# Kernel optimization log

Hardware: AMD Instinct MI355X
Metric: run time of the kernel (lower is better)

Reference implementation:

```python
import jax, jax.numpy as jnp
import numpy as np

N = 30000   # total nodes
E = 240000  # edges
B = 64      # graphs / proteins
H = 10      # GATv2 heads
C = 78      # per-head out dim (= xd_features)
D = H * C   # 780
SEQ = 1000
EMB = 128
LH = 64     # LSTM hidden per direction


def _lstm_dir(xs, Wih, Whh, bih, bhh, reverse):
    # xs: [T, Bn, EMB]; PyTorch gate order i,f,g,o
    Bn = xs.shape[1]
    h0 = jnp.zeros((Bn, LH), xs.dtype)
    def step(carry, xt):
        h, c = carry
        z = xt @ Wih.T + h @ Whh.T + bih + bhh
        i, f, g, o = jnp.split(z, 4, axis=-1)
        c = jax.nn.sigmoid(f) * c + jax.nn.sigmoid(i) * jnp.tanh(g)
        h = jax.nn.sigmoid(o) * jnp.tanh(c)
        return (h, c), h
    _, hs = jax.lax.scan(step, (h0, h0), xs, reverse=reverse)
    return hs


def setup_inputs() -> dict:
    k = jax.random.key(0)
    nxt = lambda i: jax.random.fold_in(k, i)
    s = 0.05
    d = {}
    d['x'] = jax.random.normal(nxt(0), (N, C), jnp.float32)
    d['edge_index'] = jax.random.randint(nxt(1), (2, E), 0, N)
    d['batch'] = jnp.sort(jax.random.randint(nxt(2), (N,), 0, B))
    d['target'] = jax.random.randint(nxt(3), (B, SEQ), 0, 26)
    # GATv2Conv params (share_weights=False)
    d['Wl'] = jax.random.normal(nxt(4), (C, D), jnp.float32) * s
    d['Wr'] = jax.random.normal(nxt(5), (C, D), jnp.float32) * s
    d['att'] = jax.random.normal(nxt(6), (H, C), jnp.float32) * s
    d['gat_b'] = jnp.zeros((D,), jnp.float32)
    # GCNConv params
    d['gcn_w'] = jax.random.normal(nxt(7), (D, D), jnp.float32) * s
    d['gcn_b'] = jnp.zeros((D,), jnp.float32)
    # protein branch
    d['emb'] = jax.random.normal(nxt(8), (26, EMB), jnp.float32) * s
    for tag, base in (('f', 9), ('b', 13)):
        d['Wih_' + tag] = jax.random.normal(nxt(base), (4 * LH, EMB), jnp.float32) * s
        d['Whh_' + tag] = jax.random.normal(nxt(base + 1), (4 * LH, LH), jnp.float32) * s
        d['bih_' + tag] = jnp.zeros((4 * LH,), jnp.float32)
        d['bhh_' + tag] = jnp.zeros((4 * LH,), jnp.float32)
    d['conv_w'] = jax.random.normal(nxt(17), (32, SEQ, 8), jnp.float32) * s
    d['conv_b'] = jnp.zeros((32,), jnp.float32)
    d['fcp_w'] = jax.random.normal(nxt(18), (32 * 121, 128), jnp.float32) * s
    d['fcp_b'] = jnp.zeros((128,), jnp.float32)
    # combined MLP (actual concat dim = 2*780 + 128 = 1688)
    d['fc1_w'] = jax.random.normal(nxt(19), (1688, 1024), jnp.float32) * s
    d['fc1_b'] = jnp.zeros((1024,), jnp.float32)
    d['fc2_w'] = jax.random.normal(nxt(20), (1024, 512), jnp.float32) * s
    d['fc2_b'] = jnp.zeros((512,), jnp.float32)
    d['out_w'] = jax.random.normal(nxt(21), (512, 1), jnp.float32) * s
    d['out_b'] = jnp.zeros((1,), jnp.float32)
    return d


def reference(x, edge_index, batch, target, Wl, Wr, att, gat_b, gcn_w, gcn_b,
              emb, Wih_f, Whh_f, bih_f, bhh_f, Wih_b, Whh_b, bih_b, bhh_b,
              conv_w, conv_b, fcp_w, fcp_b, fc1_w, fc1_b, fc2_w, fc2_b,
              out_w, out_b):
    # ---- graph branch (eval mode: dropout off) ----
    loops = jnp.arange(N)
    src = jnp.concatenate([edge_index[0], loops])  # self loops (PyG default)
    dst = jnp.concatenate([edge_index[1], loops])

    # GATv2Conv
    xl = (x @ Wl).reshape(N, H, C)
    xr = (x @ Wr).reshape(N, H, C)
    e = jax.nn.leaky_relu(xl[src] + xr[dst], 0.2)       # [E+N, H, C]
    logit = jnp.einsum('ehc,hc->eh', e, att)            # [E+N, H]
    m = jax.ops.segment_max(logit, dst, num_segments=N)
    ex = jnp.exp(logit - m[dst])
    den = jax.ops.segment_sum(ex, dst, num_segments=N)
    alpha = ex / den[dst]
    h = jax.ops.segment_sum(alpha[:, :, None] * xl[src], dst, num_segments=N)
    h = jax.nn.elu(h.reshape(N, D) + gat_b)

    # GCNConv with symmetric normalization
    hw = h @ gcn_w
    deg = jax.ops.segment_sum(jnp.ones_like(src, jnp.float32), dst, num_segments=N)
    dinv = jnp.where(deg > 0, jax.lax.rsqrt(jnp.maximum(deg, 1e-12)), 0.0)
    norm = dinv[src] * dinv[dst]
    g = jax.ops.segment_sum(norm[:, None] * hw[src], dst, num_segments=N) + gcn_b
    g = jax.nn.relu(g)

    # global max + mean pooling per graph
    gmax = jax.ops.segment_max(g, batch, num_segments=B)
    cnt = jax.ops.segment_sum(jnp.ones((N,), jnp.float32), batch, num_segments=B)
    gmean = jax.ops.segment_sum(g, batch, num_segments=B) / jnp.maximum(cnt, 1.0)[:, None]
    graph_feat = jnp.concatenate([gmax, gmean], axis=1)  # [B, 1560]

    # ---- protein branch ----
    et = emb[target]                                     # [B, SEQ, EMB]
    # nn.LSTM default batch_first=False: time axis is axis 0 (=B), batch axis is SEQ
    hf = _lstm_dir(et, Wih_f, Whh_f, bih_f, bhh_f, reverse=False)
    hb = _lstm_dir(et, Wih_b, Whh_b, bih_b, bhh_b, reverse=True)
    hcat = jnp.concatenate([hf, hb], axis=-1)            # [B, SEQ, 128]
    conv = jax.lax.conv_general_dilated(hcat, conv_w, (1,), 'VALID',
                                        dimension_numbers=('NCH', 'OIH', 'NCH'))
    conv = conv + conv_b[None, :, None]                  # [B, 32, 121]
    prot = conv.reshape(B, 32 * 121) @ fcp_w + fcp_b     # [B, 128]

    # ---- combined head ----
    comb = jnp.concatenate([graph_feat, prot], axis=1)   # [B, 1688]
    h1 = jax.nn.relu(comb @ fc1_w + fc1_b)
    h2 = jax.nn.relu(h1 @ fc2_w + fc2_b)
    return h2 @ out_w + out_b                            # [B, 1]
```

## Files before the change

### kernel.cpp

```cpp
#include <hip/hip_runtime.h>
#include <hip/hip_bf16.h>
#include <math.h>

static constexpr int NN   = 30000;
static constexpr int EE   = 240000;
static constexpr int ET   = EE + NN;
static constexpr int BB   = 64;
static constexpr int HH   = 10;
static constexpr int CC   = 78;
static constexpr int DD   = HH * CC;
static constexpr int SEQ  = 1000;
static constexpr int EMB  = 128;
static constexpr int LH   = 64;
static constexpr int COMBD = 2 * DD + 128;
static constexpr int PCHUNK = 64;

typedef __attribute__((ext_vector_type(8))) short short8;
typedef __attribute__((ext_vector_type(4))) float f32x4;

__device__ __forceinline__ float bf2f(unsigned short u) {
    return __uint_as_float(((unsigned int)u) << 16);
}

__device__ __forceinline__ float fast_sigmoid(float x) {
    return __builtin_amdgcn_rcpf(1.f + __expf(-x));
}
__device__ __forceinline__ float fast_tanh(float x) {
    float e = __expf(2.f * x);
    return 1.f - 2.f * __builtin_amdgcn_rcpf(e + 1.f);
}

template <int OBF>
__global__ __launch_bounds__(256) void gemm_bf16_mfma(const __hip_bfloat16* __restrict__ A,
                                                      const __hip_bfloat16* __restrict__ Bt,
                                                      void* __restrict__ Cv,
                                                      int M, int N, int K) {
    constexpr int LDS_S = 40;
    __shared__ unsigned short As[128 * LDS_S];
    __shared__ unsigned short Bs[128 * LDS_S];
    const int tid  = threadIdx.x;
    const int lane = tid & 63, wid = tid >> 6;
    const int wr = wid >> 1, wc = wid & 1;
    const int l15 = lane & 15, l4 = lane >> 4;
    int l = blockIdx.y * gridDim.x + blockIdx.x;
    {
        int nwg = gridDim.x * gridDim.y;
        int q = nwg >> 3, r = nwg & 7;
        int xcd = l & 7, idx = l >> 3;
        l = (xcd < r) ? (xcd * (q + 1) + idx) : (r * (q + 1) + (xcd - r) * q + idx);
    }
    const int bm = (l / gridDim.x) * 128;
    const int bn = (l % gridDim.x) * 128;
    const int tr = tid >> 2, tc = (tid & 3) * 8;

    const unsigned short* Au = (const unsigned short*)A;
    const unsigned short* Bu = (const unsigned short*)Bt;

    f32x4 acc[4][4];
#pragma unroll
    for (int m = 0; m < 4; ++m)
#pragma unroll
        for (int n = 0; n < 4; ++n) acc[m][n] = (f32x4){0.f, 0.f, 0.f, 0.f};

    for (int k0 = 0; k0 < K; k0 += 32) {
#pragma unroll
        for (int half = 0; half < 2; ++half) {
            int row = tr + half * 64;
            {
                int grow = bm + row;
                short8 sv;
                if (grow < M && k0 + tc + 8 <= K) {
                    const unsigned int* p = (const unsigned int*)(Au + (size_t)grow * K + k0 + tc);
#pragma unroll
                    for (int j = 0; j < 4; ++j) {
                        unsigned int u = p[j];
                        sv[2 * j]     = (short)(u & 0xffffu);
                        sv[2 * j + 1] = (short)(u >> 16);
                    }
                } else {
#pragma unroll
                    for (int j = 0; j < 8; ++j) {
                        int gk = k0 + tc + j;
                        sv[j] = (grow < M && gk < K) ? (short)Au[(size_t)grow * K + gk] : (short)0;
                    }
                }
                *reinterpret_cast<short8*>(&As[row * LDS_S + tc]) = sv;
            }
            {
                int grow = bn + row;
                short8 sv;
                if (grow < N && k0 + tc + 8 <= K) {
                    const unsigned int* p = (const unsigned int*)(Bu + (size_t)grow * K + k0 + tc);
#pragma unroll
                    for (int j = 0; j < 4; ++j) {
                        unsigned int u = p[j];
                        sv[2 * j]     = (short)(u & 0xffffu);
                        sv[2 * j + 1] = (short)(u >> 16);
                    }
                } else {
#pragma unroll
                    for (int j = 0; j < 8; ++j) {
                        int gk = k0 + tc + j;
                        sv[j] = (grow < N && gk < K) ? (short)Bu[(size_t)grow * K + gk] : (short)0;
                    }
                }
                *reinterpret_cast<short8*>(&Bs[row * LDS_S + tc]) = sv;
            }
        }
        __syncthreads();
        short8 a[4], b[4];
#pragma unroll
        for (int m = 0; m < 4; ++m)
            a[m] = *reinterpret_cast<const short8*>(&As[(wr * 64 + m * 16 + l15) * LDS_S + l4 * 8]);
#pragma unroll
        for (int n = 0; n < 4; ++n)
            b[n] = *reinterpret_cast<const short8*>(&Bs[(wc * 64 + n * 16 + l15) * LDS_S + l4 * 8]);
#pragma unroll
        for (int m = 0; m < 4; ++m)
#pragma unroll
            for (int n = 0; n < 4; ++n)
                acc[m][n] = __builtin_amdgcn_mfma_f32_16x16x32_bf16(a[m], b[n], acc[m][n], 0, 0, 0);
        __syncthreads();
    }
#pragma unroll
    for (int m = 0; m < 4; ++m)
#pragma unroll
        for (int n = 0; n < 4; ++n)
#pragma unroll
            for (int r = 0; r < 4; ++r) {
                int row = bm + wr * 64 + m * 16 + l4 * 4 + r;
                int col = bn + wc * 64 + n * 16 + l15;
                if (row < M && col < N) {
                    if (OBF)
                        ((__hip_bfloat16*)Cv)[(size_t)row * N + col] = __float2bfloat16(acc[m][n][r]);
                    else
                        ((float*)Cv)[(size_t)row * N + col] = acc[m][n][r];
                }
            }
}

__global__ void f32_to_bf16(const float* __restrict__ in, __hip_bfloat16* __restrict__ out, int n) {
    int i = blockIdx.x * blockDim.x + threadIdx.x;
    if (i < n) out[i] = __float2bfloat16(in[i]);
}

__global__ void transpose_to_bf16(const float* __restrict__ in, __hip_bfloat16* __restrict__ out,
                                  int Kdim, int Ndim) {
    int idx = blockIdx.x * blockDim.x + threadIdx.x;
    if (idx >= Kdim * Ndim) return;
    int n = idx / Kdim, k = idx % Kdim;
    out[idx] = __float2bfloat16(in[(size_t)k * Ndim + n]);
}

__global__ void transpose_f32(const float* __restrict__ in, float* __restrict__ out,
                              int Kdim, int Ndim) {
    int idx = blockIdx.x * blockDim.x + threadIdx.x;
    if (idx >= Kdim * Ndim) return;
    int n = idx / Kdim, k = idx % Kdim;
    out[idx] = in[(size_t)k * Ndim + n];
}

template <int ACT>
__global__ __launch_bounds__(256) void gemm_skinny(const float* __restrict__ A,
                                                   const float* __restrict__ Bt,
                                                   const float* __restrict__ bias,
                                                   float* __restrict__ C,
                                                   int M, int N, int K, int ldc) {
    int oidx = blockIdx.x * 4 + (threadIdx.x >> 6);
    int lane = threadIdx.x & 63;
    if (oidx >= M * N) return;
    int row = oidx / N, col = oidx % N;
    const float4* a = (const float4*)(A + (size_t)row * K);
    const float4* b = (const float4*)(Bt + (size_t)col * K);
    int K4 = K >> 2;
    float s = 0.f;
    for (int i = lane; i < K4; i += 64) {
        float4 x = a[i], y = b[i];
        s += x.x * y.x + x.y * y.y + x.z * y.z + x.w * y.w;
    }
#pragma unroll
    for (int off = 32; off; off >>= 1) s += __shfl_xor(s, off);
    if (lane == 0) {
        s += bias[col];
        if (ACT == 1) s = fmaxf(s, 0.f);
        C[(size_t)row * ldc + col] = s;
    }
}

__global__ void deg_count(const int* __restrict__ ei, int* __restrict__ deg) {
    int e = blockIdx.x * blockDim.x + threadIdx.x;
    if (e >= ET) return;
    int d = (e < EE) ? ei[EE + e] : (e - EE);
    atomicAdd(&deg[d], 1);
}

__global__ __launch_bounds__(1024) void scan_kernel(const int* __restrict__ deg,
                                                    int* __restrict__ offs) {
    __shared__ int lds[1024];
    int tid = threadIdx.x;
    const int chunk = (NN + 1023) / 1024;
    int base = tid * chunk;
    int s = 0;
    for (int i = 0; i < chunk; ++i) {
        int idx = base + i;
        if (idx < NN) s += deg[idx];
    }
    lds[tid] = s;
    __syncthreads();
    for (int d = 1; d < 1024; d <<= 1) {
        int v = (tid >= d) ? lds[tid - d] : 0;
        __syncthreads();
        lds[tid] += v;
        __syncthreads();
    }
    int run = (tid == 0) ? 0 : lds[tid - 1];
    for (int i = 0; i < chunk; ++i) {
        int idx = base + i;
        if (idx < NN) { offs[idx] = run; run += deg[idx]; }
    }
    if (tid == 1023) offs[NN] = lds[1023];
}

__global__ void csr_fill(const int* __restrict__ ei, const int* __restrict__ offs,
                         int* __restrict__ cursor, int* __restrict__ csr_src,
                         int* __restrict__ csr_dst) {
    int e = blockIdx.x * blockDim.x + threadIdx.x;
    if (e >= ET) return;
    int s = (e < EE) ? ei[e] : (e - EE);
    int d = (e < EE) ? ei[EE + e] : (e - EE);
    int pos = atomicAdd(&cursor[d], 1);
    int slot = offs[d] + pos;
    csr_src[slot] = s;
    csr_dst[slot] = d;
}

__global__ void dinv_kernel(const int* __restrict__ deg, float* __restrict__ dinv) {
    int n = blockIdx.x * blockDim.x + threadIdx.x;
    if (n >= NN) return;
    float dg = (float)deg[n];
    dinv[n] = (dg > 0.f) ? 1.f / sqrtf(dg) : 0.f;
}

__global__ void gat_logits(const unsigned short* __restrict__ xl,
                           const unsigned short* __restrict__ xr,
                           const float* __restrict__ att, const int* __restrict__ csr_src,
                           const int* __restrict__ csr_dst, float* __restrict__ logit) {
    int idx = blockIdx.x * blockDim.x + threadIdx.x;
    if (idx >= ET * HH) return;
    int i = idx / HH, h = idx % HH;
    int s = csr_src[i], d = csr_dst[i];
    const unsigned int* pl = (const unsigned int*)(xl + (size_t)s * DD + h * CC);
    const unsigned int* pr = (const unsigned int*)(xr + (size_t)d * DD + h * CC);
    const float* pa = att + h * CC;
    float acc = 0.f;
#pragma unroll
    for (int c = 0; c < CC / 2; ++c) {
        unsigned int a = pl[c], b = pr[c];
        float v0 = __uint_as_float((a & 0xffffu) << 16) + __uint_as_float((b & 0xffffu) << 16);
        float v1 = __uint_as_float(a & 0xffff0000u) + __uint_as_float(b & 0xffff0000u);
        v0 = (v0 > 0.f) ? v0 : 0.2f * v0;
        v1 = (v1 > 0.f) ? v1 : 0.2f * v1;
        acc += pa[2 * c] * v0 + pa[2 * c + 1] * v1;
    }
    logit[idx] = acc;
}

__global__ void gat_softmax(const int* __restrict__ offs, float* __restrict__ logit) {
    int idx = blockIdx.x * blockDim.x + threadIdx.x;
    if (idx >= NN * HH) return;
    int n = idx / HH, h = idx % HH;
    int i0 = offs[n], i1 = offs[n + 1];
    float m = -1e30f;
    for (int i = i0; i < i1; ++i) m = fmaxf(m, logit[i * HH + h]);
    float den = 0.f;
    for (int i = i0; i < i1; ++i) {
        float e = __expf(logit[i * HH + h] - m);
        logit[i * HH + h] = e;
        den += e;
    }
    float inv = __builtin_amdgcn_rcpf(den);
    for (int i = i0; i < i1; ++i) logit[i * HH + h] *= inv;
}

__global__ __launch_bounds__(256) void gat_aggregate(const int* __restrict__ offs,
                                                     const int* __restrict__ csr_src,
                                                     const float* __restrict__ alpha,
                                                     const unsigned short* __restrict__ xl,
                                                     const float* __restrict__ gat_b,
                                                     __hip_bfloat16* __restrict__ hout) {
    int n = blockIdx.x;
    int tid = threadIdx.x;
    int i0 = offs[n], i1 = offs[n + 1];
    int d0 = tid, d1 = tid + 256, d2 = tid + 512, d3 = tid + 768;
    int h0 = d0 / CC, h1 = d1 / CC, h2 = d2 / CC, h3 = (d3 < DD) ? d3 / CC : 0;
    float a0 = 0.f, a1 = 0.f, a2 = 0.f, a3 = 0.f;
    for (int i = i0; i < i1; ++i) {
        const unsigned short* row = xl + (size_t)csr_src[i] * DD;
        const float* al = alpha + (size_t)i * HH;
        a0 += al[h0] * bf2f(row[d0]);
        a1 += al[h1] * bf2f(row[d1]);
        a2 += al[h2] * bf2f(row[d2]);
        if (d3 < DD) a3 += al[h3] * bf2f(row[d3]);
    }
    float v;
    v = a0 + gat_b[d0]; v = (v > 0.f) ? v : expf(v) - 1.f;
    hout[(size_t)n * DD + d0] = __float2bfloat16(v);
    v = a1 + gat_b[d1]; v = (v > 0.f) ? v : expf(v) - 1.f;
    hout[(size_t)n * DD + d1] = __float2bfloat16(v);
    v = a2 + gat_b[d2]; v = (v > 0.f) ? v : expf(v) - 1.f;
    hout[(size_t)n * DD + d2] = __float2bfloat16(v);
    if (d3 < DD) {
        v = a3 + gat_b[d3]; v = (v > 0.f) ? v : expf(v) - 1.f;
        hout[(size_t)n * DD + d3] = __float2bfloat16(v);
    }
}

__global__ __launch_bounds__(256) void gcn_aggregate(const int* __restrict__ offs,
                                                     const int* __restrict__ csr_src,
                                                     const float* __restrict__ dinv,
                                                     const unsigned short* __restrict__ hw,
                                                     const float* __restrict__ gcn_b,
                                                     __hip_bfloat16* __restrict__ g) {
    int n = blockIdx.x;
    int tid = threadIdx.x;
    float din = dinv[n];
    int i0 = offs[n], i1 = offs[n + 1];
    int d0 = tid, d1 = tid + 256, d2 = tid + 512, d3 = tid + 768;
    float a0 = 0.f, a1 = 0.f, a2 = 0.f, a3 = 0.f;
    for (int i = i0; i < i1; ++i) {
        int s = csr_src[i];
        float w = dinv[s] * din;
        const unsigned short* row = hw + (size_t)s * DD;
        a0 += w * bf2f(row[d0]);
        a1 += w * bf2f(row[d1]);
        a2 += w * bf2f(row[d2]);
        if (d3 < DD) a3 += w * bf2f(row[d3]);
    }
    g[(size_t)n * DD + d0] = __float2bfloat16(fmaxf(a0 + gcn_b[d0], 0.f));
    g[(size_t)n * DD + d1] = __float2bfloat16(fmaxf(a1 + gcn_b[d1], 0.f));
    g[(size_t)n * DD + d2] = __float2bfloat16(fmaxf(a2 + gcn_b[d2], 0.f));
    if (d3 < DD) g[(size_t)n * DD + d3] = __float2bfloat16(fmaxf(a3 + gcn_b[d3], 0.f));
}

__global__ void graph_ranges(const int* __restrict__ batch, int* __restrict__ gstart,
                             int* __restrict__ gend) {
    int n = blockIdx.x * blockDim.x + threadIdx.x;
    if (n >= NN) return;
    int b = batch[n];
    if (n == 0 || batch[n - 1] != b) gstart[b] = n;
    if (n == NN - 1 || batch[n + 1] != b) gend[b] = n + 1;
}

__global__ __launch_bounds__(256) void pool_partial(const unsigned short* __restrict__ g,
                                                    const int* __restrict__ batch,
                                                    float* __restrict__ pmax,
                                                    float* __restrict__ psum) {
    int chunk0 = blockIdx.x * PCHUNK;
    int tid = threadIdx.x;
    __shared__ int bsh[PCHUNK];
    for (int i = tid; i < PCHUNK; i += 256) {
        int n = chunk0 + i;
        bsh[i] = (n < NN) ? batch[n] : -1;
    }
    __syncthreads();
    float mx[4] = {0.f, 0.f, 0.f, 0.f};
    float sm[4] = {0.f, 0.f, 0.f, 0.f};
    int curb = bsh[0];
    auto flush = [&](int b) {
#pragma unroll
        for (int j = 0; j < 4; ++j) {
            int d = tid + j * 256;
            if (d < DD && b >= 0) {
                atomicMax((unsigned int*)&pmax[(size_t)b * DD + d], __float_as_uint(mx[j]));
                atomicAdd(&psum[(size_t)b * DD + d], sm[j]);
            }
            mx[j] = 0.f; sm[j] = 0.f;
        }
    };
    for (int i = 0; i < PCHUNK; ++i) {
        int n = chunk0 + i;
        if (n >= NN) break;
        int b = bsh[i];
        if (b != curb) { flush(curb); curb = b; }
        const unsigned short* row = g + (size_t)n * DD;
#pragma unroll
        for (int j = 0; j < 4; ++j) {
            int d = tid + j * 256;
            if (d < DD) {
                float v = bf2f(row[d]);
                mx[j] = fmaxf(mx[j], v);
                sm[j] += v;
            }
        }
    }
    flush(curb);
}

__global__ void pool_finalize(const float* __restrict__ pmax, const float* __restrict__ psum,
                              const int* __restrict__ gstart, const int* __restrict__ gend,
                              float* __restrict__ comb) {
    int idx = blockIdx.x * blockDim.x + threadIdx.x;
    if (idx >= BB * DD) return;
    int b = idx / DD, d = idx % DD;
    float cnt = fmaxf((float)(gend[b] - gstart[b]), 1.f);
    comb[(size_t)b * COMBD + d] = pmax[idx];
    comb[(size_t)b * COMBD + DD + d] = psum[idx] / cnt;
}

__global__ void proj26_kernel(const float* __restrict__ emb,
                              const float* __restrict__ Wih_f, const float* __restrict__ bih_f,
                              const float* __restrict__ bhh_f,
                              const float* __restrict__ Wih_b, const float* __restrict__ bih_b,
                              const float* __restrict__ bhh_b, float* __restrict__ proj) {
    int dir = blockIdx.x, row = blockIdx.y, j = threadIdx.x;
    const float* W = dir ? Wih_b : Wih_f;
    const float* b1 = dir ? bih_b : bih_f;
    const float* b2 = dir ? bhh_b : bhh_f;
    float acc = b1[j] + b2[j];
    const float* e = emb + row * EMB;
    const float* w = W + j * EMB;
    for (int k = 0; k < EMB; ++k) acc += e[k] * w[k];
    proj[(dir * 26 + row) * 256 + j] = acc;
}

__global__ __launch_bounds__(256) void lstm_kernel(const int* __restrict__ target,
                                                   const float* __restrict__ proj26,
                                                   const float* __restrict__ Whh_f,
                                                   const float* __restrict__ Whh_b,
                                                   float* __restrict__ hcat) {
    int n = blockIdx.x;
    int dir = blockIdx.y;
    int tid = threadIdx.x;
    const float* Whh = dir ? Whh_b : Whh_f;
    const float* proj = proj26 + dir * 26 * 256;
    const int gate = tid >> 6;
    float w[LH];
#pragma unroll
    for (int u4 = 0; u4 < LH / 4; ++u4) {
        float4 v = *reinterpret_cast<const float4*>(Whh + tid * LH + u4 * 4);
        w[u4 * 4 + 0] = v.x; w[u4 * 4 + 1] = v.y;
        w[u4 * 4 + 2] = v.z; w[u4 * 4 + 3] = v.w;
    }
    __shared__ float h_lds[LH];
    __shared__ float z_lds[256];
    float c_reg = 0.f;
    if (tid < LH) h_lds[tid] = 0.f;
    __syncthreads();
    for (int s = 0; s < BB; ++s) {
        int t = dir ? (BB - 1 - s) : s;
        int tgt = target[t * SEQ + n];
        float a0 = 0.f, a1 = 0.f, a2 = 0.f, a3 = 0.f;
#pragma unroll
        for (int u = 0; u < LH; u += 4) {
            a0 += w[u] * h_lds[u];
            a1 += w[u + 1] * h_lds[u + 1];
            a2 += w[u + 2] * h_lds[u + 2];
            a3 += w[u + 3] * h_lds[u + 3];
        }
        float z = proj[tgt * 256 + tid] + a0 + a1 + a2 + a3;
        z_lds[tid] = (gate == 2) ? fast_tanh(z) : fast_sigmoid(z);
        __syncthreads();
        if (tid < LH) {
            float ig = z_lds[tid];
            float fg = z_lds[LH + tid];
            float gg = z_lds[2 * LH + tid];
            float og = z_lds[3 * LH + tid];
            float c = fg * c_reg + ig * gg;
            float h = og * fast_tanh(c);
            c_reg = c;
            h_lds[tid] = h;
            hcat[((size_t)t * SEQ + n) * 128 + dir * LH + tid] = h;
        }
        __syncthreads();
    }
}

__global__ __launch_bounds__(256) void transpose_hcat(const float* __restrict__ hcat,
                                                      unsigned short* __restrict__ hcatT) {
    int b = blockIdx.z;
    int i0 = blockIdx.y * 32;
    int h0 = blockIdx.x * 32;
    int th = threadIdx.x & 31;
    int ti = threadIdx.x >> 5;
    __shared__ float t[32][33];
#pragma unroll
    for (int r = 0; r < 4; ++r) {
        int i = i0 + ti + r * 8;
        if (i < SEQ) t[ti + r * 8][th] = hcat[((size_t)b * SEQ + i) * 128 + h0 + th];
    }
    __syncthreads();
#pragma unroll
    for (int r = 0; r < 4; ++r) {
        int h = h0 + ti + r * 8;
        int i = i0 + th;
        if (i < SEQ) {
            unsigned int u = __float_as_uint(t[th][ti + r * 8]);
            unsigned int lsb = (u >> 16) & 1u;
            u += 0x7fffu + lsb;
            hcatT[((size_t)b * 128 + h) * SEQ + i] = (unsigned short)(u >> 16);
        }
    }
}

__global__ void reshape_convw(const float* __restrict__ conv_w, __hip_bfloat16* __restrict__ wT) {
    int idx = blockIdx.x * blockDim.x + threadIdx.x;
    if (idx >= 256 * SEQ) return;
    int np = idx / SEQ, i = idx % SEQ;
    int o = np >> 3, k = np & 7;
    wT[idx] = __float2bfloat16(conv_w[((size_t)o * SEQ + i) * 8 + k]);
}

__global__ void conv_finalize(const float* __restrict__ T, const float* __restrict__ conv_b,
                              float* __restrict__ convout) {
    int idx = blockIdx.x * blockDim.x + threadIdx.x;
    if (idx >= BB * 32 * 121) return;
    int p = idx % 121;
    int o = (idx / 121) % 32;
    int b = idx / (121 * 32);
    float acc = conv_b[o];
#pragma unroll
    for (int k = 0; k < 8; ++k)
        acc += T[(size_t)(b * 128 + p + k) * 256 + o * 8 + k];
    convout[(size_t)b * 3872 + o * 121 + p] = acc;
}

extern "C" void kernel_launch(void* const* d_in, const int* in_sizes, int n_in,
                              void* d_out, int out_size, void* d_ws, size_t ws_size,
                              hipStream_t stream) {
    const float* x      = (const float*)d_in[0];
    const int*   ei     = (const int*)d_in[1];
    const int*   batch  = (const int*)d_in[2];
    const int*   target = (const int*)d_in[3];
    const float* Wl     = (const float*)d_in[4];
    const float* Wr     = (const float*)d_in[5];
    const float* att    = (const float*)d_in[6];
    const float* gat_b  = (const float*)d_in[7];
    const float* gcn_w  = (const float*)d_in[8];
    const float* gcn_b  = (const float*)d_in[9];
    const float* emb    = (const float*)d_in[10];
    const float* Wih_f  = (const float*)d_in[11];
    const float* Whh_f  = (const float*)d_in[12];
    const float* bih_f  = (const float*)d_in[13];
    const float* bhh_f  = (const float*)d_in[14];
    const float* Wih_b  = (const float*)d_in[15];
    const float* Whh_b  = (const float*)d_in[16];
    const float* bih_b  = (const float*)d_in[17];
    const float* bhh_b  = (const float*)d_in[18];
    const float* conv_w = (const float*)d_in[19];
    const float* conv_b = (const float*)d_in[20];
    const float* fcp_w  = (const float*)d_in[21];
    const float* fcp_b  = (const float*)d_in[22];
    const float* fc1_w  = (const float*)d_in[23];
    const float* fc1_b  = (const float*)d_in[24];
    const float* fc2_w  = (const float*)d_in[25];
    const float* fc2_b  = (const float*)d_in[26];
    const float* out_w  = (const float*)d_in[27];
    const float* out_b  = (const float*)d_in[28];
    float* out = (float*)d_out;
    (void)n_in; (void)in_sizes; (void)out_size;

    char* ws = (char*)d_ws;
    size_t o = 0;
    auto alloc = [&](size_t bytes) {
        char* p = ws + o;
        o = (o + bytes + 255) & ~(size_t)255;
        return p;
    };
    constexpr size_t HALF = (size_t)NN * DD * 2;
    char* region = (char*)alloc(2 * HALF);
    __hip_bfloat16* xl_bf = (__hip_bfloat16*)region;
    __hip_bfloat16* xr_bf = (__hip_bfloat16*)(region + HALF);
    __hip_bfloat16* hw_bf = (__hip_bfloat16*)region;
    __hip_bfloat16* g_bf  = (__hip_bfloat16*)(region + HALF);
    char* rp = region;
    auto palloc = [&](size_t bytes) {
        char* p = rp;
        rp += (bytes + 255) & ~(size_t)255;
        return p;
    };
    float* hcat    = (float*)palloc((size_t)BB * SEQ * 128 * 4);
    float* proj26  = (float*)palloc(2 * 26 * 256 * 4);
    float* convout = (float*)palloc((size_t)BB * 3872 * 4);
    __hip_bfloat16* wT = (__hip_bfloat16*)palloc((size_t)256 * SEQ * 2);
    unsigned short* hcatT = (unsigned short*)palloc((size_t)BB * 128 * SEQ * 2);
    float* T = (float*)palloc((size_t)BB * 128 * 256 * 4);
    __hip_bfloat16* h_bf  = (__hip_bfloat16*)alloc(HALF);
    __hip_bfloat16* x_bf  = (__hip_bfloat16*)alloc((size_t)NN * CC * 2);
    __hip_bfloat16* wl_t  = (__hip_bfloat16*)alloc((size_t)DD * CC * 2);
    __hip_bfloat16* wr_t  = (__hip_bfloat16*)alloc((size_t)DD * CC * 2);
    __hip_bfloat16* gcw_t = (__hip_bfloat16*)alloc((size_t)DD * DD * 2);
    float* fcp_wt = (float*)alloc((size_t)3872 * 128 * 4);
    float* fc1_wt = (float*)alloc((size_t)COMBD * 1024 * 4);
    float* fc2_wt = (float*)alloc((size_t)1024 * 512 * 4);
    float* out_wt = (float*)alloc((size_t)512 * 4);
    float* logit    = (float*)alloc((size_t)ET * HH * 4);
    int*   csr_src  = (int*)alloc((size_t)ET * 4);
    int*   csr_dst  = (int*)alloc((size_t)ET * 4);
    int*   deg      = (int*)alloc((size_t)NN * 4);
    int*   cursor   = (int*)alloc((size_t)NN * 4);
    int*   offs     = (int*)alloc((size_t)(NN + 1) * 4);
    float* dinv     = (float*)alloc((size_t)NN * 4);
    int*   gstart   = (int*)alloc(64 * 4);
    int*   gend     = (int*)alloc(64 * 4);
    float* pmax     = (float*)alloc((size_t)BB * DD * 4);
    float* psum     = (float*)alloc((size_t)BB * DD * 4);
    float* comb     = (float*)alloc((size_t)BB * COMBD * 4);
    float* h1       = (float*)alloc((size_t)BB * 1024 * 4);
    float* h2       = (float*)alloc((size_t)BB * 512 * 4);
    if (o > ws_size) return;

    hipMemsetAsync(deg, 0, (size_t)NN * 4, stream);
    hipMemsetAsync(cursor, 0, (size_t)NN * 4, stream);
    hipMemsetAsync(gstart, 0, 64 * 4, stream);
    hipMemsetAsync(gend, 0, 64 * 4, stream);
    hipMemsetAsync(pmax, 0, (size_t)BB * DD * 4, stream);
    hipMemsetAsync(psum, 0, (size_t)BB * DD * 4, stream);

    {
        dim3 grid(2, 26);
        proj26_kernel<<<grid, 256, 0, stream>>>(emb, Wih_f, bih_f, bhh_f, Wih_b, bih_b, bhh_b, proj26);
    }
    {
        dim3 grid(SEQ, 2);
        lstm_kernel<<<grid, 256, 0, stream>>>(target, proj26, Whh_f, Whh_b, hcat);
    }
    {
        dim3 grid(4, 32, BB);
        transpose_hcat<<<grid, 256, 0, stream>>>(hcat, hcatT);
    }
    reshape_convw<<<(256 * SEQ + 255) / 256, 256, 0, stream>>>(conv_w, wT);
    {
        dim3 grid(2, 64);
        gemm_bf16_mfma<0><<<grid, 256, 0, stream>>>((const __hip_bfloat16*)hcatT, wT, T,
                                                    BB * 128, 256, SEQ);
    }
    conv_finalize<<<(BB * 32 * 121 + 255) / 256, 256, 0, stream>>>(T, conv_b, convout);
    transpose_f32<<<(3872 * 128 + 255) / 256, 256, 0, stream>>>(fcp_w, fcp_wt, 3872, 128);
    gemm_skinny<0><<<(BB * 128 + 3) / 4, 256, 0, stream>>>(convout, fcp_wt, fcp_b,
                                                           comb + 2 * DD, BB, 128, 3872, COMBD);

    f32_to_bf16<<<(NN * CC + 255) / 256, 256, 0, stream>>>(x, x_bf, NN * CC);
    transpose_to_bf16<<<(CC * DD + 255) / 256, 256, 0, stream>>>(Wl, wl_t, CC, DD);
    transpose_to_bf16<<<(CC * DD + 255) / 256, 256, 0, stream>>>(Wr, wr_t, CC, DD);
    transpose_to_bf16<<<(DD * DD + 255) / 256, 256, 0, stream>>>(gcn_w, gcw_t, DD, DD);
    transpose_f32<<<(COMBD * 1024 + 255) / 256, 256, 0, stream>>>(fc1_w, fc1_wt, COMBD, 1024);
    transpose_f32<<<(1024 * 512 + 255) / 256, 256, 0, stream>>>(fc2_w, fc2_wt, 1024, 512);
    transpose_f32<<<(512 + 255) / 256, 256, 0, stream>>>(out_w, out_wt, 512, 1);

    dim3 ggrid((DD + 127) / 128, (NN + 127) / 128);
    gemm_bf16_mfma<1><<<ggrid, 256, 0, stream>>>(x_bf, wl_t, xl_bf, NN, DD, CC);
    gemm_bf16_mfma<1><<<ggrid, 256, 0, stream>>>(x_bf, wr_t, xr_bf, NN, DD, CC);
    deg_count<<<(ET + 255) / 256, 256, 0, stream>>>(ei, deg);
    scan_kernel<<<1, 1024, 0, stream>>>(deg, offs);
    csr_fill<<<(ET + 255) / 256, 256, 0, stream>>>(ei, offs, cursor, csr_src, csr_dst);
    dinv_kernel<<<(NN + 255) / 256, 256, 0, stream>>>(deg, dinv);
    gat_logits<<<(ET * HH + 255) / 256, 256, 0, stream>>>((const unsigned short*)xl_bf,
                                                          (const unsigned short*)xr_bf,
                                                          att, csr_src, csr_dst, logit);
    gat_softmax<<<(NN * HH + 255) / 256, 256, 0, stream>>>(offs, logit);
    gat_aggregate<<<NN, 256, 0, stream>>>(offs, csr_src, logit,
                                          (const unsigned short*)xl_bf, gat_b, h_bf);
    gemm_bf16_mfma<1><<<ggrid, 256, 0, stream>>>(h_bf, gcw_t, hw_bf, NN, DD, DD);
    gcn_aggregate<<<NN, 256, 0, stream>>>(offs, csr_src, dinv,
                                          (const unsigned short*)hw_bf, gcn_b, g_bf);
    graph_ranges<<<(NN + 255) / 256, 256, 0, stream>>>(batch, gstart, gend);
    pool_partial<<<(NN + PCHUNK - 1) / PCHUNK, 256, 0, stream>>>((const unsigned short*)g_bf,
                                                                 batch, pmax, psum);
    pool_finalize<<<(BB * DD + 255) / 256, 256, 0, stream>>>(pmax, psum, gstart, gend, comb);

    gemm_skinny<1><<<(BB * 1024 + 3) / 4, 256, 0, stream>>>(comb, fc1_wt, fc1_b, h1,
                                                            BB, 1024, COMBD, 1024);
    gemm_skinny<1><<<(BB * 512 + 3) / 4, 256, 0, stream>>>(h1, fc2_wt, fc2_b, h2,
                                                           BB, 512, 1024, 512);
    gemm_skinny<0><<<(BB + 3) / 4, 256, 0, stream>>>(h2, out_wt, out_b, out,
                                                     BB, 1, 512, 1);
}
```

Before: 960.9 us.

## Pad per-head features to 80 columns for vectorized bf16 gathers

```diff
diff --git a/kernel.cpp b/kernel.cpp
--- a/kernel.cpp
+++ b/kernel.cpp
@@ -8,7 +8,9 @@
 static constexpr int BB   = 64;
 static constexpr int HH   = 10;
 static constexpr int CC   = 78;
+static constexpr int CCP  = 80;
 static constexpr int DD   = HH * CC;
+static constexpr int DDP  = HH * CCP;
 static constexpr int SEQ  = 1000;
 static constexpr int EMB  = 128;
 static constexpr int LH   = 64;
@@ -21,7 +23,18 @@
 __device__ __forceinline__ float bf2f(unsigned short u) {
     return __uint_as_float(((unsigned int)u) << 16);
 }
-
+__device__ __forceinline__ float bflo(unsigned int u) {
+    return __uint_as_float(u << 16);
+}
+__device__ __forceinline__ float bfhi(unsigned int u) {
+    return __uint_as_float(u & 0xffff0000u);
+}
+__device__ __forceinline__ unsigned int pack2bf(float x, float y) {
+    __hip_bfloat16 bx = __float2bfloat16(x), by = __float2bfloat16(y);
+    unsigned short ux = *reinterpret_cast<unsigned short*>(&bx);
+    unsigned short uy = *reinterpret_cast<unsigned short*>(&by);
+    return (unsigned int)ux | ((unsigned int)uy << 16);
+}
 __device__ __forceinline__ float fast_sigmoid(float x) {
     return __builtin_amdgcn_rcpf(1.f + __expf(-x));
 }
@@ -30,11 +43,11 @@
     return 1.f - 2.f * __builtin_amdgcn_rcpf(e + 1.f);
 }
 
-template <int OBF>
+template <int OBF, int PADHEAD>
 __global__ __launch_bounds__(256) void gemm_bf16_mfma(const __hip_bfloat16* __restrict__ A,
                                                       const __hip_bfloat16* __restrict__ Bt,
                                                       void* __restrict__ Cv,
-                                                      int M, int N, int K) {
+                                                      int M, int N, int K, int ldc) {
     constexpr int LDS_S = 40;
     __shared__ unsigned short As[128 * LDS_S];
     __shared__ unsigned short Bs[128 * LDS_S];
@@ -131,10 +144,11 @@
                 int row = bm + wr * 64 + m * 16 + l4 * 4 + r;
                 int col = bn + wc * 64 + n * 16 + l15;
                 if (row < M && col < N) {
+                    int pc = PADHEAD ? ((col / CC) * CCP + (col % CC)) : col;
                     if (OBF)
-                        ((__hip_bfloat16*)Cv)[(size_t)row * N + col] = __float2bfloat16(acc[m][n][r]);
+                        ((__hip_bfloat16*)Cv)[(size_t)row * ldc + pc] = __float2bfloat16(acc[m][n][r]);
                     else
-                        ((float*)Cv)[(size_t)row * N + col] = acc[m][n][r];
+                        ((float*)Cv)[(size_t)row * ldc + pc] = acc[m][n][r];
                 }
             }
 }
@@ -158,6 +172,22 @@
     if (idx >= Kdim * Ndim) return;
     int n = idx / Kdim, k = idx % Kdim;
     out[idx] = in[(size_t)k * Ndim + n];
+}
+
+__global__ void pad_att(const float* __restrict__ att, float* __restrict__ att_p) {
+    int idx = blockIdx.x * blockDim.x + threadIdx.x;
+    if (idx >= HH * CCP) return;
+    int h = idx / CCP, c = idx % CCP;
+    att_p[idx] = (c < CC) ? att[h * CC + c] : 0.f;
+}
+
+__global__ void zero_pads(unsigned int* __restrict__ a, unsigned int* __restrict__ b) {
+    int idx = blockIdx.x * blockDim.x + threadIdx.x;
+    if (idx >= NN * HH) return;
+    int n = idx / HH, h = idx % HH;
+    size_t p = ((size_t)n * DDP + h * CCP + CC) >> 1;
+    a[p] = 0u;
+    b[p] = 0u;
 }
 
 template <int ACT>
@@ -241,26 +271,34 @@
     dinv[n] = (dg > 0.f) ? 1.f / sqrtf(dg) : 0.f;
 }
 
+__device__ __forceinline__ float dot2lr(unsigned int a, unsigned int b, float w0, float w1) {
+    float v0 = bflo(a) + bflo(b);
+    float v1 = bfhi(a) + bfhi(b);
+    v0 = (v0 > 0.f) ? v0 : 0.2f * v0;
+    v1 = (v1 > 0.f) ? v1 : 0.2f * v1;
+    return w0 * v0 + w1 * v1;
+}
+
 __global__ void gat_logits(const unsigned short* __restrict__ xl,
                            const unsigned short* __restrict__ xr,
-                           const float* __restrict__ att, const int* __restrict__ csr_src,
+                           const float* __restrict__ att_p, const int* __restrict__ csr_src,
                            const int* __restrict__ csr_dst, float* __restrict__ logit) {
     int idx = blockIdx.x * blockDim.x + threadIdx.x;
     if (idx >= ET * HH) return;
     int i = idx / HH, h = idx % HH;
     int s = csr_src[i], d = csr_dst[i];
-    const unsigned int* pl = (const unsigned int*)(xl + (size_t)s * DD + h * CC);
-    const unsigned int* pr = (const unsigned int*)(xr + (size_t)d * DD + h * CC);
-    const float* pa = att + h * CC;
+    const uint4* pl = (const uint4*)(xl + (size_t)s * DDP + h * CCP);
+    const uint4* pr = (const uint4*)(xr + (size_t)d * DDP + h * CCP);
+    const float* pa = att_p + h * CCP;
     float acc = 0.f;
 #pragma unroll
-    for (int c = 0; c < CC / 2; ++c) {
-        unsigned int a = pl[c], b = pr[c];
-        float v0 = __uint_as_float((a & 0xffffu) << 16) + __uint_as_float((b & 0xffffu) << 16);
-        float v1 = __uint_as_float(a & 0xffff0000u) + __uint_as_float(b & 0xffff0000u);
-        v0 = (v0 > 0.f) ? v0 : 0.2f * v0;
-        v1 = (v1 > 0.f) ? v1 : 0.2f * v1;
-        acc += pa[2 * c] * v0 + pa[2 * c + 1] * v1;
+    for (int q = 0; q < CCP / 8; ++q) {
+        uint4 a = pl[q], b = pr[q];
+        const float* p8 = pa + q * 8;
+        acc += dot2lr(a.x, b.x, p8[0], p8[1]);
+        acc += dot2lr(a.y, b.y, p8[2], p8[3]);
+        acc += dot2lr(a.z, b.z, p8[4], p8[5]);
+        acc += dot2lr(a.w, b.w, p8[6], p8[7]);
     }
     logit[idx] = acc;
 }
@@ -285,61 +323,92 @@
 __global__ __launch_bounds__(256) void gat_aggregate(const int* __restrict__ offs,
                                                      const int* __restrict__ csr_src,
                                                      const float* __restrict__ alpha,
-                                                     const unsigned short* __restrict__ xl,
+                                                     const unsigned int* __restrict__ xl,
                                                      const float* __restrict__ gat_b,
-                                                     __hip_bfloat16* __restrict__ hout) {
+                                                     unsigned int* __restrict__ hout) {
     int n = blockIdx.x;
     int tid = threadIdx.x;
     int i0 = offs[n], i1 = offs[n + 1];
-    int d0 = tid, d1 = tid + 256, d2 = tid + 512, d3 = tid + 768;
-    int h0 = d0 / CC, h1 = d1 / CC, h2 = d2 / CC, h3 = (d3 < DD) ? d3 / CC : 0;
-    float a0 = 0.f, a1 = 0.f, a2 = 0.f, a3 = 0.f;
+    const int U = DDP / 2;
+    int u0 = tid, u1 = tid + 256;
+    bool v1 = (u1 < U);
+    int h0 = u0 / (CCP / 2), h1 = v1 ? u1 / (CCP / 2) : 0;
+    float lo0 = 0.f, hi0 = 0.f, lo1 = 0.f, hi1 = 0.f;
     for (int i = i0; i < i1; ++i) {
-        const unsigned short* row = xl + (size_t)csr_src[i] * DD;
+        const unsigned int* row = xl + (size_t)csr_src[i] * U;
         const float* al = alpha + (size_t)i * HH;
-        a0 += al[h0] * bf2f(row[d0]);
-        a1 += al[h1] * bf2f(row[d1]);
-        a2 += al[h2] * bf2f(row[d2]);
-        if (d3 < DD) a3 += al[h3] * bf2f(row[d3]);
-    }
-    float v;
-    v = a0 + gat_b[d0]; v = (v > 0.f) ? v : expf(v) - 1.f;
-    hout[(size_t)n * DD + d0] = __float2bfloat16(v);
-    v = a1 + gat_b[d1]; v = (v > 0.f) ? v : expf(v) - 1.f;
-    hout[(size_t)n * DD + d1] = __float2bfloat16(v);
-    v = a2 + gat_b[d2]; v = (v > 0.f) ? v : expf(v) - 1.f;
-    hout[(size_t)n * DD + d2] = __float2bfloat16(v);
-    if (d3 < DD) {
-        v = a3 + gat_b[d3]; v = (v > 0.f) ? v : expf(v) - 1.f;
-        hout[(size_t)n * DD + d3] = __float2bfloat16(v);
+        unsigned int w0 = row[u0];
+        float p0 = al[h0];
+        lo0 += p0 * bflo(w0);
+        hi0 += p0 * bfhi(w0);
+        if (v1) {
+            unsigned int w1 = row[u1];
+            float p1 = al[h1];
+            lo1 += p1 * bflo(w1);
+            hi1 += p1 * bfhi(w1);
+        }
+    }
+    int m0 = u0 % (CCP / 2);
+    if (m0 != (CCP / 2 - 1)) {
+        int d = h0 * CC + 2 * m0;
+        float x = lo0 + gat_b[d];     x = (x > 0.f) ? x : __expf(x) - 1.f;
+        float y = hi0 + gat_b[d + 1]; y = (y > 0.f) ? y : __expf(y) - 1.f;
+        hout[((size_t)n * DD + d) >> 1] = pack2bf(x, y);
+    }
+    if (v1) {
+        int m1 = u1 % (CCP / 2);
+        if (m1 != (CCP / 2 - 1)) {
+            int d = h1 * CC + 2 * m1;
+            float x = lo1 + gat_b[d];     x = (x > 0.f) ? x : __expf(x) - 1.f;
+            float y = hi1 + gat_b[d + 1]; y = (y > 0.f) ? y : __expf(y) - 1.f;
+            hout[((size_t)n * DD + d) >> 1] = pack2bf(x, y);
+        }
     }
 }
 
 __global__ __launch_bounds__(256) void gcn_aggregate(const int* __restrict__ offs,
                                                      const int* __restrict__ csr_src,
                                                      const float* __restrict__ dinv,
-                                                     const unsigned short* __restrict__ hw,
+                                                     const unsigned int* __restrict__ hw,
                                                      const float* __restrict__ gcn_b,
-                                                     __hip_bfloat16* __restrict__ g) {
+                                                     unsigned int* __restrict__ g) {
     int n = blockIdx.x;
     int tid = threadIdx.x;
     float din = dinv[n];
     int i0 = offs[n], i1 = offs[n + 1];
-    int d0 = tid, d1 = tid + 256, d2 = tid + 512, d3 = tid + 768;
-    float a0 = 0.f, a1 = 0.f, a2 = 0.f, a3 = 0.f;
+    const int U = DDP / 2;
+    int u0 = tid, u1 = tid + 256;
+    bool v1 = (u1 < U);
+    float lo0 = 0.f, hi0 = 0.f, lo1 = 0.f, hi1 = 0.f;
     for (int i = i0; i < i1; ++i) {
         int s = csr_src[i];
         float w = dinv[s] * din;
-        const unsigned short* row = hw + (size_t)s * DD;
-        a0 += w * bf2f(row[d0]);
-        a1 += w * bf2f(row[d1]);
-        a2 += w * bf2f(row[d2]);
-        if (d3 < DD) a3 += w * bf2f(row[d3]);
-    }
-    g[(size_t)n * DD + d0] = __float2bfloat16(fmaxf(a0 + gcn_b[d0], 0.f));
-    g[(size_t)n * DD + d1] = __float2bfloat16(fmaxf(a1 + gcn_b[d1], 0.f));
-    g[(size_t)n * DD + d2] = __float2bfloat16(fmaxf(a2 + gcn_b[d2], 0.f));
-    if (d3 < DD) g[(size_t)n * DD + d3] = __float2bfloat16(fmaxf(a3 + gcn_b[d3], 0.f));
+        const unsigned int* row = hw + (size_t)s * U;
+        unsigned int w0 = row[u0];
+        lo0 += w * bflo(w0);
+        hi0 += w * bfhi(w0);
+        if (v1) {
+            unsigned int w1 = row[u1];
+            lo1 += w * bflo(w1);
+            hi1 += w * bfhi(w1);
+        }
+    }
+    int m0 = u0 % (CCP / 2);
+    if (m0 != (CCP / 2 - 1)) {
+        int d = (u0 / (CCP / 2)) * CC + 2 * m0;
+        float x = fmaxf(lo0 + gcn_b[d], 0.f);
+        float y = fmaxf(hi0 + gcn_b[d + 1], 0.f);
+        g[(size_t)n * U + u0] = pack2bf(x, y);
+    }
+    if (v1) {
+        int m1 = u1 % (CCP / 2);
+        if (m1 != (CCP / 2 - 1)) {
+            int d = (u1 / (CCP / 2)) * CC + 2 * m1;
+            float x = fmaxf(lo1 + gcn_b[d], 0.f);
+            float y = fmaxf(hi1 + gcn_b[d + 1], 0.f);
+            g[(size_t)n * U + u1] = pack2bf(x, y);
+        }
+    }
 }
 
 __global__ void graph_ranges(const int* __restrict__ batch, int* __restrict__ gstart,
@@ -351,7 +420,7 @@
     if (n == NN - 1 || batch[n + 1] != b) gend[b] = n + 1;
 }
 
-__global__ __launch_bounds__(256) void pool_partial(const unsigned short* __restrict__ g,
+__global__ __launch_bounds__(256) void pool_partial(const unsigned int* __restrict__ g,
                                                     const int* __restrict__ batch,
                                                     float* __restrict__ pmax,
                                                     float* __restrict__ psum) {
@@ -363,34 +432,51 @@
         bsh[i] = (n < NN) ? batch[n] : -1;
     }
     __syncthreads();
-    float mx[4] = {0.f, 0.f, 0.f, 0.f};
-    float sm[4] = {0.f, 0.f, 0.f, 0.f};
+    const int U = DDP / 2;
+    int u0 = tid, u1 = tid + 256;
+    bool v1 = (u1 < U);
+    float mA = 0.f, mB = 0.f, mC = 0.f, mD = 0.f;
+    float sA = 0.f, sB = 0.f, sC = 0.f, sD = 0.f;
     int curb = bsh[0];
     auto flush = [&](int b) {
-#pragma unroll
-        for (int j = 0; j < 4; ++j) {
-            int d = tid + j * 256;
-            if (d < DD && b >= 0) {
-                atomicMax((unsigned int*)&pmax[(size_t)b * DD + d], __float_as_uint(mx[j]));
-                atomicAdd(&psum[(size_t)b * DD + d], sm[j]);
+        if (b >= 0) {
+            int m0 = u0 % (CCP / 2);
+            if (m0 != (CCP / 2 - 1)) {
+                int d = (u0 / (CCP / 2)) * CC + 2 * m0;
+                atomicMax((unsigned int*)&pmax[(size_t)b * DD + d], __float_as_uint(mA));
+                atomicAdd(&psum[(size_t)b * DD + d], sA);
+                atomicMax((unsigned int*)&pmax[(size_t)b * DD + d + 1], __float_as_uint(mB));
+                atomicAdd(&psum[(size_t)b * DD + d + 1], sB);
             }
-            mx[j] = 0.f; sm[j] = 0.f;
-        }
+            if (v1) {
+                int m1 = u1 % (CCP / 2);
+                if (m1 != (CCP / 2 - 1)) {
+                    int d = (u1 / (CCP / 2)) * CC + 2 * m1;
+                    atomicMax((unsigned int*)&pmax[(size_t)b * DD + d], __float_as_uint(mC));
+                    atomicAdd(&psum[(size_t)b * DD + d], sC);
+                    atomicMax((unsigned int*)&pmax[(size_t)b * DD + d + 1], __float_as_uint(mD));
+                    atomicAdd(&psum[(size_t)b * DD + d + 1], sD);
+                }
+            }
+        }
+        mA = mB = mC = mD = 0.f;
+        sA = sB = sC = sD = 0.f;
     };
     for (int i = 0; i < PCHUNK; ++i) {
         int n = chunk0 + i;
         if (n >= NN) break;
         int b = bsh[i];
         if (b != curb) { flush(curb); curb = b; }
-        const unsigned short* row = g + (size_t)n * DD;
-#pragma unroll
-        for (int j = 0; j < 4; ++j) {
-            int d = tid + j * 256;
-            if (d < DD) {
-                float v = bf2f(row[d]);
-                mx[j] = fmaxf(mx[j], v);
-                sm[j] += v;
-            }
+        const unsigned int* row = g + (size_t)n * U;
+        unsigned int w0 = row[u0];
+        float x = bflo(w0), y = bfhi(w0);
+        mA = fmaxf(mA, x); sA += x;
+        mB = fmaxf(mB, y); sB += y;
+        if (v1) {
+            unsigned int w1 = row[u1];
+            float z = bflo(w1), t = bfhi(w1);
+            mC = fmaxf(mC, z); sC += z;
+            mD = fmaxf(mD, t); sD += t;
         }
     }
     flush(curb);
@@ -566,7 +652,7 @@
         o = (o + bytes + 255) & ~(size_t)255;
         return p;
     };
-    constexpr size_t HALF = (size_t)NN * DD * 2;
+    constexpr size_t HALF = (size_t)NN * DDP * 2;
     char* region = (char*)alloc(2 * HALF);
     __hip_bfloat16* xl_bf = (__hip_bfloat16*)region;
     __hip_bfloat16* xr_bf = (__hip_bfloat16*)(region + HALF);
@@ -584,11 +670,12 @@
     __hip_bfloat16* wT = (__hip_bfloat16*)palloc((size_t)256 * SEQ * 2);
     unsigned short* hcatT = (unsigned short*)palloc((size_t)BB * 128 * SEQ * 2);
     float* T = (float*)palloc((size_t)BB * 128 * 256 * 4);
-    __hip_bfloat16* h_bf  = (__hip_bfloat16*)alloc(HALF);
+    __hip_bfloat16* h_bf  = (__hip_bfloat16*)alloc((size_t)NN * DD * 2);
     __hip_bfloat16* x_bf  = (__hip_bfloat16*)alloc((size_t)NN * CC * 2);
     __hip_bfloat16* wl_t  = (__hip_bfloat16*)alloc((size_t)DD * CC * 2);
     __hip_bfloat16* wr_t  = (__hip_bfloat16*)alloc((size_t)DD * CC * 2);
     __hip_bfloat16* gcw_t = (__hip_bfloat16*)alloc((size_t)DD * DD * 2);
+    float* att_p  = (float*)alloc((size_t)HH * CCP * 4);
     float* fcp_wt = (float*)alloc((size_t)3872 * 128 * 4);
     float* fc1_wt = (float*)alloc((size_t)COMBD * 1024 * 4);
     float* fc2_wt = (float*)alloc((size_t)1024 * 512 * 4);
@@ -631,8 +718,8 @@
     reshape_convw<<<(256 * SEQ + 255) / 256, 256, 0, stream>>>(conv_w, wT);
     {
         dim3 grid(2, 64);
-        gemm_bf16_mfma<0><<<grid, 256, 0, stream>>>((const __hip_bfloat16*)hcatT, wT, T,
-                                                    BB * 128, 256, SEQ);
+        gemm_bf16_mfma<0, 0><<<grid, 256, 0, stream>>>((const __hip_bfloat16*)hcatT, wT, T,
+                                                       BB * 128, 256, SEQ, 256);
     }
     conv_finalize<<<(BB * 32 * 121 + 255) / 256, 256, 0, stream>>>(T, conv_b, convout);
     transpose_f32<<<(3872 * 128 + 255) / 256, 256, 0, stream>>>(fcp_w, fcp_wt, 3872, 128);
@@ -643,28 +730,32 @@
     transpose_to_bf16<<<(CC * DD + 255) / 256, 256, 0, stream>>>(Wl, wl_t, CC, DD);
     transpose_to_bf16<<<(CC * DD + 255) / 256, 256, 0, stream>>>(Wr, wr_t, CC, DD);
     transpose_to_bf16<<<(DD * DD + 255) / 256, 256, 0, stream>>>(gcn_w, gcw_t, DD, DD);
+    pad_att<<<(HH * CCP + 255) / 256, 256, 0, stream>>>(att, att_p);
     transpose_f32<<<(COMBD * 1024 + 255) / 256, 256, 0, stream>>>(fc1_w, fc1_wt, COMBD, 1024);
     transpose_f32<<<(1024 * 512 + 255) / 256, 256, 0, stream>>>(fc2_w, fc2_wt, 1024, 512);
     transpose_f32<<<(512 + 255) / 256, 256, 0, stream>>>(out_w, out_wt, 512, 1);
 
     dim3 ggrid((DD + 127) / 128, (NN + 127) / 128);
-    gemm_bf16_mfma<1><<<ggrid, 256, 0, stream>>>(x_bf, wl_t, xl_bf, NN, DD, CC);
-    gemm_bf16_mfma<1><<<ggrid, 256, 0, stream>>>(x_bf, wr_t, xr_bf, NN, DD, CC);
+    gemm_bf16_mfma<1, 1><<<ggrid, 256, 0, stream>>>(x_bf, wl_t, xl_bf, NN, DD, CC, DDP);
+    gemm_bf16_mfma<1, 1><<<ggrid, 256, 0, stream>>>(x_bf, wr_t, xr_bf, NN, DD, CC, DDP);
+    zero_pads<<<(NN * HH + 255) / 256, 256, 0, stream>>>((unsigned int*)xl_bf, (unsigned int*)xr_bf);
     deg_count<<<(ET + 255) / 256, 256, 0, stream>>>(ei, deg);
     scan_kernel<<<1, 1024, 0, stream>>>(deg, offs);
     csr_fill<<<(ET + 255) / 256, 256, 0, stream>>>(ei, offs, cursor, csr_src, csr_dst);
     dinv_kernel<<<(NN + 255) / 256, 256, 0, stream>>>(deg, dinv);
     gat_logits<<<(ET * HH + 255) / 256, 256, 0, stream>>>((const unsigned short*)xl_bf,
                                                           (const unsigned short*)xr_bf,
-                                                          att, csr_src, csr_dst, logit);
+                                                          att_p, csr_src, csr_dst, logit);
     gat_softmax<<<(NN * HH + 255) / 256, 256, 0, stream>>>(offs, logit);
     gat_aggregate<<<NN, 256, 0, stream>>>(offs, csr_src, logit,
-                                          (const unsigned short*)xl_bf, gat_b, h_bf);
-    gemm_bf16_mfma<1><<<ggrid, 256, 0, stream>>>(h_bf, gcw_t, hw_bf, NN, DD, DD);
+                                          (const unsigned int*)xl_bf, gat_b,
+                                          (unsigned int*)h_bf);
+    gemm_bf16_mfma<1, 1><<<ggrid, 256, 0, stream>>>(h_bf, gcw_t, hw_bf, NN, DD, DD, DDP);
     gcn_aggregate<<<NN, 256, 0, stream>>>(offs, csr_src, dinv,
-                                          (const unsigned short*)hw_bf, gcn_b, g_bf);
+                                          (const unsigned int*)hw_bf, gcn_b,
+                                          (unsigned int*)g_bf);
     graph_ranges<<<(NN + 255) / 256, 256, 0, stream>>>(batch, gstart, gend);
-    pool_partial<<<(NN + PCHUNK - 1) / PCHUNK, 256, 0, stream>>>((const unsigned short*)g_bf,
+    pool_partial<<<(NN + PCHUNK - 1) / PCHUNK, 256, 0, stream>>>((const unsigned int*)g_bf,
                                                                  batch, pmax, psum);
     pool_finalize<<<(BB * DD + 255) / 256, 256, 0, stream>>>(pmax, psum, gstart, gend, comb);
 
```

New measurement: 941.8 us. 2.0% less time.
